# Kernel optimization log

Hardware: AMD Instinct MI355X
Metric: run time of the kernel (lower is better)

Reference implementation:

```python
import jax, jax.numpy as jnp
import numpy as np
import math

H = 16  # heads
EPS_NORM = 1e-12
EPS_W = 1e-6


def setup_inputs() -> dict:
    key = jax.random.key(0)
    ks = jax.random.split(key, 6)
    B, T, d = 2, 2048, 1024
    s = 1.0 / math.sqrt(d)
    return {
        "x": jax.random.normal(ks[0], (B, T, d), dtype=jnp.float32),
        "Wq": jax.random.normal(ks[1], (d, d), dtype=jnp.float32) * s,
        "Wk": jax.random.normal(ks[2], (d, d), dtype=jnp.float32) * s,
        "Wv": jax.random.normal(ks[3], (d, d), dtype=jnp.float32) * s,
        "Wo": jax.random.normal(ks[4], (d, d), dtype=jnp.float32) * s,
        "bo": jnp.zeros((d,), dtype=jnp.float32),
    }


def _l2norm(t):
    # F.normalize(dim=-1): x / max(||x||, eps)
    n = jnp.sqrt(jnp.sum(t * t, axis=-1, keepdims=True))
    return t / jnp.maximum(n, EPS_NORM)


def reference(x, Wq, Wk, Wv, Wo, bo):
    B, T, d = x.shape
    dk = d // H
    # projections (torch Linear: y = x @ W.T), split heads -> [B, H, T, dk]
    def proj(W):
        return (x @ W.T).reshape(B, T, H, dk).transpose(0, 2, 1, 3)
    Q = _l2norm(proj(Wq))
    K = _l2norm(proj(Wk))
    V = proj(Wv)
    # angular similarity scores [B, H, T, T]
    sim = jnp.clip(jnp.einsum("bhqd,bhkd->bhqk", Q, K), -0.999, 0.999)
    scores = 1.0 - jnp.arccos(sim) / jnp.float32(math.pi)
    W = jnp.maximum(scores, EPS_W) ** 8
    W = W / (jnp.sum(W, axis=-1, keepdims=True) + EPS_W)
    out = jnp.einsum("bhqk,bhkd->bhqd", W, V)  # [B, H, T, dk]
    out = out.transpose(0, 2, 1, 3).reshape(B, T, d)
    return out @ Wo.T + bo
```

## Files before the change

kernel.cpp:

```cpp
#include <hip/hip_runtime.h>
#include <hip/hip_bf16.h>
#include <hip/hip_fp16.h>
#include <math.h>

#define BB 2
#define TT 2048
#define DD 1024
#define HH 16
#define DK 64
#define KT 64

typedef _Float16 f16x8 __attribute__((ext_vector_type(8)));
typedef __fp16 fp16x2 __attribute__((ext_vector_type(2)));
typedef __attribute__((ext_vector_type(4))) float f32x4;
typedef __attribute__((ext_vector_type(2))) float f32x2;

static __device__ __forceinline__ void g2lds16(const void* g, void* l) {
    __builtin_amdgcn_global_load_lds(
        (const __attribute__((address_space(1))) unsigned int*)g,
        (__attribute__((address_space(3))) unsigned int*)l, 16, 0, 0);
}

static __device__ __forceinline__ f32x2 w8pair(f32x2 s, f32x2& rs) {
    f32x2 ax;
    ax.x = fminf(fabsf(s.x), 0.999f);
    ax.y = fminf(fabsf(s.y), 0.999f);
    f32x2 p = ax * -0.0059617f + 0.0236380f;
    p = p * ax + (-0.0675180f);
    p = p * ax + 0.49997851f;
    f32x2 om = 1.0f - ax;
    f32x2 u;
    u.x = sqrtf(om.x);
    u.y = sqrtf(om.y);
    f32x2 uq = u * p;
    f32x2 e = 0.5f - uq;
    f32x2 t;
    t.x = 0.5f + copysignf(e.x, s.x);
    t.y = 0.5f + copysignf(e.y, s.y);
    f32x2 t2 = t * t;
    f32x2 t4 = t2 * t2;
    f32x2 t8 = t4 * t4;
    rs += t8;
    return t8;
}
static __device__ __forceinline__ int packh2(f32x2 v) {
    union { fp16x2 h; int i; } u;
    u.h = __builtin_amdgcn_cvt_pkrtz(v.x, v.y);
    return u.i;
}

__global__ __launch_bounds__(256) void cvtall_kernel(
    const float* __restrict__ x,  const float* __restrict__ Wq,
    const float* __restrict__ Wk, const float* __restrict__ Wv,
    const float* __restrict__ Wo,
    _Float16* __restrict__ xh, _Float16* __restrict__ W3h,
    _Float16* __restrict__ Woh)
{
    const int bid = blockIdx.x;
    const float* s; _Float16* d; int blk;
    if (bid < 2048) { s = x; d = xh; blk = bid; }
    else {
        const int idx = bid - 2048;
        const int w   = idx >> 9;
        blk = idx & 511;
        s = (w == 0) ? Wq : (w == 1) ? Wk : (w == 2) ? Wv : Wo;
        d = (w == 3) ? Woh : W3h + (size_t)w * (DD * DD);
    }
    const int i = (blk * 256 + threadIdx.x) * 8;
    float4 a = *(const float4*)(s + i);
    float4 b = *(const float4*)(s + i + 4);
    union { _Float16 h[8]; int4 v; } u;
    u.h[0] = (_Float16)a.x; u.h[1] = (_Float16)a.y;
    u.h[2] = (_Float16)a.z; u.h[3] = (_Float16)a.w;
    u.h[4] = (_Float16)b.x; u.h[5] = (_Float16)b.y;
    u.h[6] = (_Float16)b.z; u.h[7] = (_Float16)b.w;
    *(int4*)(d + i) = u.v;
}

template<int NPROD, int EPI>
__global__ __launch_bounds__(256, NPROD == 1 ? 3 : 2) void gemm_f16_128(
    const _Float16* __restrict__ Ah_g, const _Float16* __restrict__ Al_g,
    const _Float16* __restrict__ B_g, const float* __restrict__ bias,
    float* __restrict__ C,
    _Float16* __restrict__ Qh, _Float16* __restrict__ Kh,
    _Float16* __restrict__ Vh,
    int nbx, int K, int hasBias)
{
    __shared__ _Float16 Ahs[8][128][8];
    __shared__ _Float16 Bhs[8][128][8];
    __shared__ _Float16 Als[NPROD == 2 ? 8 : 1][128][8];

    const int nwg  = gridDim.x;
    const int wgid = blockIdx.x;
    const int cpx  = nwg >> 3;
    const int swz  = (wgid & 7) * cpx + (wgid >> 3);
    const int by   = swz / nbx;
    const int bx   = swz - by * nbx;

    const int t    = threadIdx.x;
    const int m0   = by * 128;
    const int n0g  = bx * 128;
    const int seg  = n0g >> 10;
    const int n0   = n0g & 1023;

    const int lane = t & 63;
    const int w    = t >> 6;
    const int wm   = w >> 1;
    const int wn   = w & 1;
    const int l15  = lane & 15;
    const int quad = lane >> 4;

    f32x4 acc[4][4];
#pragma unroll
    for (int i = 0; i < 4; ++i)
#pragma unroll
        for (int j = 0; j < 4; ++j) acc[i][j] = (f32x4)0.f;

    for (int k0 = 0; k0 < K; k0 += 64) {
        __syncthreads();
#pragma unroll
        for (int i = 0; i < 2; ++i) {
            const int cc = w * 2 + i;
#pragma unroll
            for (int half = 0; half < 2; ++half) {
                g2lds16(Ah_g + (size_t)(m0 + half * 64 + lane) * K + k0 + cc * 8,
                        &Ahs[cc][half * 64][0]);
                if (NPROD == 2)
                    g2lds16(Al_g + (size_t)(m0 + half * 64 + lane) * K + k0 + cc * 8,
                            &Als[cc][half * 64][0]);
                g2lds16(B_g + (size_t)(n0g + half * 64 + lane) * K + k0 + cc * 8,
                        &Bhs[cc][half * 64][0]);
            }
        }
        __syncthreads();

#pragma unroll
        for (int kh = 0; kh < 2; ++kh) {
            f16x8 ah[4], bh[4];
#pragma unroll
            for (int tm = 0; tm < 4; ++tm)
                ah[tm] = *(const f16x8*)&Ahs[kh * 4 + quad][wm * 64 + tm * 16 + l15][0];
#pragma unroll
            for (int tn = 0; tn < 4; ++tn)
                bh[tn] = *(const f16x8*)&Bhs[kh * 4 + quad][wn * 64 + tn * 16 + l15][0];
#pragma unroll
            for (int tm = 0; tm < 4; ++tm)
#pragma unroll
                for (int tn = 0; tn < 4; ++tn)
                    acc[tm][tn] = __builtin_amdgcn_mfma_f32_16x16x32_f16(
                        ah[tm], bh[tn], acc[tm][tn], 0, 0, 0);
            if (NPROD == 2) {
                f16x8 al[4];
#pragma unroll
                for (int tm = 0; tm < 4; ++tm)
                    al[tm] = *(const f16x8*)&Als[kh * 4 + quad][wm * 64 + tm * 16 + l15][0];
#pragma unroll
                for (int tm = 0; tm < 4; ++tm)
#pragma unroll
                    for (int tn = 0; tn < 4; ++tn)
                        acc[tm][tn] = __builtin_amdgcn_mfma_f32_16x16x32_f16(
                            al[tm], bh[tn], acc[tm][tn], 0, 0, 0);
            }
        }
    }

    if (EPI == 0) {
#pragma unroll
        for (int tm = 0; tm < 4; ++tm)
#pragma unroll
            for (int tn = 0; tn < 4; ++tn) {
                const int col  = n0 + wn * 64 + tn * 16 + l15;
                const float bv = hasBias ? bias[col] : 0.f;
                const int rowb = m0 + wm * 64 + tm * 16 + quad * 4;
#pragma unroll
                for (int r = 0; r < 4; ++r)
                    C[(size_t)(rowb + r) * 1024 + col] = acc[tm][tn][r] + bv;
            }
    } else {
        if (seg < 2) {
            _Float16* __restrict__ dstb = (seg == 0) ? Qh : Kh;
            const int hh = (n0 >> 6) + wn;
#pragma unroll
            for (int tm = 0; tm < 4; ++tm) {
#pragma unroll
                for (int r = 0; r < 4; ++r) {
                    float ss = 0.f;
#pragma unroll
                    for (int tn = 0; tn < 4; ++tn) {
                        const float v = acc[tm][tn][r];
                        ss += v * v;
                    }
                    ss += __shfl_xor(ss, 1);
                    ss += __shfl_xor(ss, 2);
                    ss += __shfl_xor(ss, 4);
                    ss += __shfl_xor(ss, 8);
                    const float inv = rsqrtf(fmaxf(ss, 1e-24f));
                    const int row = m0 + wm * 64 + tm * 16 + quad * 4 + r;
                    const int b   = row >> 11;
                    const int tt  = row & 2047;
                    _Float16* dst = dstb + ((size_t)(b * HH + hh) * TT + tt) * DK;
#pragma unroll
                    for (int tn = 0; tn < 4; ++tn)
                        dst[tn * 16 + l15] = (_Float16)(acc[tm][tn][r] * inv);
                }
            }
        } else {
#pragma unroll
            for (int tm = 0; tm < 4; ++tm)
#pragma unroll
                for (int tn = 0; tn < 4; ++tn) {
                    const int col  = n0 + wn * 64 + tn * 16 + l15;
                    const int rowb = m0 + wm * 64 + tm * 16 + quad * 4;
#pragma unroll
                    for (int r = 0; r < 4; ++r)
                        Vh[(size_t)(rowb + r) * 1024 + col] =
                            (_Float16)acc[tm][tn][r];
                }
        }
    }
}

__global__ __launch_bounds__(256) void vtrans_kernel(
    const _Float16* __restrict__ Vh, _Float16* __restrict__ Vt)
{
    __shared__ _Float16 Vtmp[64][72];
    const int t  = threadIdx.x;
    const int t0 = blockIdx.x * 64;
    const int h  = blockIdx.y;
    const int b  = blockIdx.z;

    {
        const int i  = t >> 2;
        const int jc = (t & 3) * 16;
        const _Float16* src = Vh + (size_t)(b * TT + t0 + i) * DD + h * DK + jc;
        f16x8 a = *(const f16x8*)(src);
        f16x8 c = *(const f16x8*)(src + 8);
#pragma unroll
        for (int e = 0; e < 8; ++e) {
            Vtmp[jc + e][i]     = a[e];
            Vtmp[jc + 8 + e][i] = c[e];
        }
    }
    __syncthreads();
    {
        const int d  = t >> 2;
        const int kc = (t & 3) * 16;
        _Float16* dst = Vt + ((size_t)((b * HH + h) * DK + d)) * TT + t0 + kc;
        *(int4*)(dst)     = *(const int4*)&Vtmp[d][kc];
        *(int4*)(dst + 8) = *(const int4*)&Vtmp[d][kc + 8];
    }
}

__global__ __launch_bounds__(256, 4) void attn_kernel(
    const _Float16* __restrict__ Qh_g, const _Float16* __restrict__ Kh_g,
    const _Float16* __restrict__ Vt_g,
    _Float16* __restrict__ Oh, _Float16* __restrict__ Ol)
{
    __shared__ _Float16 Vts[2][8][64][8];
    __shared__ _Float16 Ws[2][64][72];
    __shared__ float Rbuf[4][64];
    __shared__ float Rfin[64];

    const int t    = threadIdx.x;
    const int lane = t & 63;
    const int w    = t >> 6;
    const int l15  = lane & 15;
    const int quad = lane >> 4;
    const int q0   = blockIdx.x * 64;
    const int h    = blockIdx.y;
    const int b    = blockIdx.z;
    const size_t bh = (size_t)(b * HH + h);

    const _Float16* kh_g = Kh_g + bh * TT * DK;
    const _Float16* vt_g = Vt_g + bh * (size_t)DK * TT;

    f16x8 qf[4][2];
#pragma unroll
    for (int qt = 0; qt < 4; ++qt)
#pragma unroll
        for (int s = 0; s < 2; ++s)
            qf[qt][s] = *(const f16x8*)(Qh_g + (bh * TT + q0 + qt * 16 + l15) * DK
                                        + s * 32 + quad * 8);

    f16x8 kf[2], kfn[2];
#pragma unroll
    for (int s = 0; s < 2; ++s) {
        kf[s] = *(const f16x8*)(kh_g
            + (size_t)(w * 16 + l15) * DK + s * 32 + quad * 8);
        kfn[s] = kf[s];
    }

#pragma unroll
    for (int j = 0; j < 2; ++j) {
        const int kc = w * 2 + j;
        g2lds16(vt_g + (size_t)lane * TT + kc * 8, &Vts[0][kc][0][0]);
    }

    f32x4 acc[4];
#pragma unroll
    for (int j = 0; j < 4; ++j) acc[j] = (f32x4)0.f;
    f32x2 rs2[4];
#pragma unroll
    for (int j = 0; j < 4; ++j) rs2[j] = (f32x2)0.f;

    int p = 0;
    for (int k0 = 0; k0 < TT; k0 += KT, p ^= 1) {
        const int kn = k0 + KT;
        if (kn < TT) {
#pragma unroll
            for (int s = 0; s < 2; ++s)
                kfn[s] = *(const f16x8*)(kh_g
                    + (size_t)(kn + w * 16 + l15) * DK + s * 32 + quad * 8);
        }

#pragma unroll
        for (int qt = 0; qt < 4; ++qt) {
            f32x4 c_ = (f32x4)0.f;
#pragma unroll
            for (int s = 0; s < 2; ++s)
                c_ = __builtin_amdgcn_mfma_f32_16x16x32_f16(
                    kf[s], qf[qt][s], c_, 0, 0, 0);
            f32x2 p01, p23;
            p01.x = c_[0]; p01.y = c_[1];
            p23.x = c_[2]; p23.y = c_[3];
            f32x2 w01 = w8pair(p01, rs2[qt]);
            f32x2 w23 = w8pair(p23, rs2[qt]);
            int2 pk;
            pk.x = packh2(w01);
            pk.y = packh2(w23);
            *(int2*)&Ws[p][qt * 16 + l15][w * 16 + quad * 4] = pk;
        }
        __syncthreads();

        if (kn < TT) {
#pragma unroll
            for (int j = 0; j < 2; ++j) {
                const int kc = w * 2 + j;
                g2lds16(vt_g + (size_t)lane * TT + kn + kc * 8,
                        &Vts[p ^ 1][kc][0][0]);
            }
        }

#pragma unroll
        for (int kstep = 0; kstep < 2; ++kstep) {
            f16x8 av = *(const f16x8*)&Ws[p][16 * w + l15][kstep * 32 + quad * 8];
#pragma unroll
            for (int nd = 0; nd < 4; ++nd) {
                f16x8 bv = *(const f16x8*)&Vts[p][kstep * 4 + quad][nd * 16 + l15][0];
                acc[nd] = __builtin_amdgcn_mfma_f32_16x16x32_f16(
                    av, bv, acc[nd], 0, 0, 0);
            }
        }

#pragma unroll
        for (int s = 0; s < 2; ++s)
            kf[s] = kfn[s];
    }

#pragma unroll
    for (int qt = 0; qt < 4; ++qt) {
        float pr = rs2[qt].x + rs2[qt].y;
        pr += __shfl_xor(pr, 16);
        pr += __shfl_xor(pr, 32);
        if (quad == 0) Rbuf[w][qt * 16 + l15] = pr;
    }
    __syncthreads();
    if (t < 64) {
        float s = Rbuf[0][t] + Rbuf[1][t] + Rbuf[2][t] + Rbuf[3][t];
        Rfin[t] = 1.f / (s + 1e-6f);
    }
    __syncthreads();

#pragma unroll
    for (int r = 0; r < 4; ++r) {
        const int q = 16 * w + quad * 4 + r;
        const float inv = Rfin[q];
        const size_t base = (size_t)(b * TT + q0 + q) * DD + h * DK + l15;
#pragma unroll
        for (int nd = 0; nd < 4; ++nd) {
            float v = acc[nd][r] * inv;
            _Float16 hv = (_Float16)v;
            Oh[base + nd * 16] = hv;
            Ol[base + nd * 16] = (_Float16)(v - (float)hv);
        }
    }
}

extern "C" void kernel_launch(void* const* d_in, const int* in_sizes, int n_in,
                              void* d_out, int out_size, void* d_ws, size_t ws_size,
                              hipStream_t stream)
{
    const float* x  = (const float*)d_in[0];
    const float* Wq = (const float*)d_in[1];
    const float* Wk = (const float*)d_in[2];
    const float* Wv = (const float*)d_in[3];
    const float* Wo = (const float*)d_in[4];
    const float* bo = (const float*)d_in[5];
    float* out = (float*)d_out;

    const int M = BB * TT;
    const int K = DD;

    const size_t MB = 1024 * 1024;
    char* ws = (char*)d_ws;
    _Float16* xh  = (_Float16*)(ws);
    _Float16* W3h = (_Float16*)(ws + 8 * MB);
    _Float16* Woh = (_Float16*)(ws + 14 * MB);
    _Float16* Qh  = (_Float16*)(ws + 16 * MB);
    _Float16* Kh  = (_Float16*)(ws + 24 * MB);
    _Float16* Vh  = (_Float16*)(ws + 32 * MB);
    _Float16* Vt  = (_Float16*)(ws + 40 * MB);
    _Float16* Oh  = (_Float16*)(ws);
    _Float16* Ol  = (_Float16*)(ws + 32 * MB);

    dim3 gB(256);

    cvtall_kernel<<<4096, gB, 0, stream>>>(x, Wq, Wk, Wv, Wo, xh, W3h, Woh);

    {
        const int nbx = 3072 / 128;
        const int nby = M / 128;
        gemm_f16_128<1, 1><<<nbx * nby, gB, 0, stream>>>(
            xh, nullptr, W3h, nullptr, nullptr, Qh, Kh, Vh, nbx, K, 0);
    }

    vtrans_kernel<<<dim3(TT / 64, HH, BB), gB, 0, stream>>>(Vh, Vt);

    attn_kernel<<<dim3(TT / 64, HH, BB), gB, 0, stream>>>(Qh, Kh, Vt, Oh, Ol);

    {
        const int nbx = 1024 / 128;
        const int nby = M / 128;
        gemm_f16_128<2, 0><<<nbx * nby, gB, 0, stream>>>(
            Oh, Ol, Woh, bo, out, nullptr, nullptr, nullptr, nbx, K, 1);
    }
}
```

Before: 310.8 us.

## Fuse V transpose into QKV GEMM epilogue and fold hi/lo split into K=2048 GEMM

The QKV GEMM epilogue now writes V directly in transposed [b,h,d,t] layout, so the separate vtrans kernel and the Vh buffer are gone. The attention output hi/lo fp16 halves are stored side by side in one [M,2048] buffer, and Wo is duplicated along K. The output projection becomes a single-product GEMM with K=2048 instead of a dual-A-operand variant. sqrt and rsqrt calls are also replaced with the AMDGCN builtins. The trade-offs are strided 8-byte V stores, twice the Wo fp16 storage, and possibly different occupancy for the output GEMM now that it uses 3 waves per SIMD.

```diff
diff --git a/kernel.cpp b/kernel.cpp
--- a/kernel.cpp
+++ b/kernel.cpp
@@ -30,8 +30,8 @@
     p = p * ax + 0.49997851f;
     f32x2 om = 1.0f - ax;
     f32x2 u;
-    u.x = sqrtf(om.x);
-    u.y = sqrtf(om.y);
+    u.x = __builtin_amdgcn_sqrtf(om.x);
+    u.y = __builtin_amdgcn_sqrtf(om.y);
     f32x2 uq = u * p;
     f32x2 e = 0.5f - uq;
     f32x2 t;
@@ -54,17 +54,16 @@
     const float* __restrict__ Wk, const float* __restrict__ Wv,
     const float* __restrict__ Wo,
     _Float16* __restrict__ xh, _Float16* __restrict__ W3h,
-    _Float16* __restrict__ Woh)
+    _Float16* __restrict__ Wo2)
 {
     const int bid = blockIdx.x;
-    const float* s; _Float16* d; int blk;
-    if (bid < 2048) { s = x; d = xh; blk = bid; }
+    const float* s; int wsel = -1, blk;
+    if (bid < 2048) { s = x; blk = bid; }
     else {
         const int idx = bid - 2048;
-        const int w   = idx >> 9;
-        blk = idx & 511;
-        s = (w == 0) ? Wq : (w == 1) ? Wk : (w == 2) ? Wv : Wo;
-        d = (w == 3) ? Woh : W3h + (size_t)w * (DD * DD);
+        wsel = idx >> 9;
+        blk  = idx & 511;
+        s = (wsel == 0) ? Wq : (wsel == 1) ? Wk : (wsel == 2) ? Wv : Wo;
     }
     const int i = (blk * 256 + threadIdx.x) * 8;
     float4 a = *(const float4*)(s + i);
@@ -74,21 +73,26 @@
     u.h[2] = (_Float16)a.z; u.h[3] = (_Float16)a.w;
     u.h[4] = (_Float16)b.x; u.h[5] = (_Float16)b.y;
     u.h[6] = (_Float16)b.z; u.h[7] = (_Float16)b.w;
-    *(int4*)(d + i) = u.v;
-}
-
-template<int NPROD, int EPI>
-__global__ __launch_bounds__(256, NPROD == 1 ? 3 : 2) void gemm_f16_128(
-    const _Float16* __restrict__ Ah_g, const _Float16* __restrict__ Al_g,
-    const _Float16* __restrict__ B_g, const float* __restrict__ bias,
-    float* __restrict__ C,
+    if (wsel < 0)      *(int4*)(xh + i) = u.v;
+    else if (wsel < 3) *(int4*)(W3h + (size_t)wsel * (DD * DD) + i) = u.v;
+    else {
+        const int n = i >> 10, k = i & 1023;
+        _Float16* dst = Wo2 + (size_t)n * 2048 + k;
+        *(int4*)dst          = u.v;
+        *(int4*)(dst + 1024) = u.v;
+    }
+}
+
+template<int EPI>
+__global__ __launch_bounds__(256, 3) void gemm_f16_128(
+    const _Float16* __restrict__ Ah_g, const _Float16* __restrict__ B_g,
+    const float* __restrict__ bias, float* __restrict__ C,
     _Float16* __restrict__ Qh, _Float16* __restrict__ Kh,
-    _Float16* __restrict__ Vh,
+    _Float16* __restrict__ Vt,
     int nbx, int K, int hasBias)
 {
     __shared__ _Float16 Ahs[8][128][8];
     __shared__ _Float16 Bhs[8][128][8];
-    __shared__ _Float16 Als[NPROD == 2 ? 8 : 1][128][8];
 
     const int nwg  = gridDim.x;
     const int wgid = blockIdx.x;
@@ -125,9 +129,6 @@
             for (int half = 0; half < 2; ++half) {
                 g2lds16(Ah_g + (size_t)(m0 + half * 64 + lane) * K + k0 + cc * 8,
                         &Ahs[cc][half * 64][0]);
-                if (NPROD == 2)
-                    g2lds16(Al_g + (size_t)(m0 + half * 64 + lane) * K + k0 + cc * 8,
-                            &Als[cc][half * 64][0]);
                 g2lds16(B_g + (size_t)(n0g + half * 64 + lane) * K + k0 + cc * 8,
                         &Bhs[cc][half * 64][0]);
             }
@@ -149,18 +150,6 @@
                 for (int tn = 0; tn < 4; ++tn)
                     acc[tm][tn] = __builtin_amdgcn_mfma_f32_16x16x32_f16(
                         ah[tm], bh[tn], acc[tm][tn], 0, 0, 0);
-            if (NPROD == 2) {
-                f16x8 al[4];
-#pragma unroll
-                for (int tm = 0; tm < 4; ++tm)
-                    al[tm] = *(const f16x8*)&Als[kh * 4 + quad][wm * 64 + tm * 16 + l15][0];
-#pragma unroll
-                for (int tm = 0; tm < 4; ++tm)
-#pragma unroll
-                    for (int tn = 0; tn < 4; ++tn)
-                        acc[tm][tn] = __builtin_amdgcn_mfma_f32_16x16x32_f16(
-                            al[tm], bh[tn], acc[tm][tn], 0, 0, 0);
-            }
         }
     }
 
@@ -194,7 +183,7 @@
                     ss += __shfl_xor(ss, 2);
                     ss += __shfl_xor(ss, 4);
                     ss += __shfl_xor(ss, 8);
-                    const float inv = rsqrtf(fmaxf(ss, 1e-24f));
+                    const float inv = __builtin_amdgcn_rsqf(fmaxf(ss, 1e-24f));
                     const int row = m0 + wm * 64 + tm * 16 + quad * 4 + r;
                     const int b   = row >> 11;
                     const int tt  = row & 2047;
@@ -205,56 +194,31 @@
                 }
             }
         } else {
-#pragma unroll
-            for (int tm = 0; tm < 4; ++tm)
-#pragma unroll
-                for (int tn = 0; tn < 4; ++tn) {
-                    const int col  = n0 + wn * 64 + tn * 16 + l15;
-                    const int rowb = m0 + wm * 64 + tm * 16 + quad * 4;
-#pragma unroll
-                    for (int r = 0; r < 4; ++r)
-                        Vh[(size_t)(rowb + r) * 1024 + col] =
-                            (_Float16)acc[tm][tn][r];
+            const int hh = (n0 >> 6) + wn;
+            const int rowb = m0 + wm * 64 + quad * 4;
+            const int bb  = rowb >> 11;
+            const int tt0 = rowb & 2047;
+#pragma unroll
+            for (int tn = 0; tn < 4; ++tn) {
+                const int d = tn * 16 + l15;
+                _Float16* dst = Vt + ((size_t)(bb * HH + hh) * DK + d) * TT;
+#pragma unroll
+                for (int tm = 0; tm < 4; ++tm) {
+                    union { _Float16 h[4]; int2 v; } uu;
+                    uu.h[0] = (_Float16)acc[tm][tn][0];
+                    uu.h[1] = (_Float16)acc[tm][tn][1];
+                    uu.h[2] = (_Float16)acc[tm][tn][2];
+                    uu.h[3] = (_Float16)acc[tm][tn][3];
+                    *(int2*)(dst + tt0 + tm * 16) = uu.v;
                 }
-        }
-    }
-}
-
-__global__ __launch_bounds__(256) void vtrans_kernel(
-    const _Float16* __restrict__ Vh, _Float16* __restrict__ Vt)
-{
-    __shared__ _Float16 Vtmp[64][72];
-    const int t  = threadIdx.x;
-    const int t0 = blockIdx.x * 64;
-    const int h  = blockIdx.y;
-    const int b  = blockIdx.z;
-
-    {
-        const int i  = t >> 2;
-        const int jc = (t & 3) * 16;
-        const _Float16* src = Vh + (size_t)(b * TT + t0 + i) * DD + h * DK + jc;
-        f16x8 a = *(const f16x8*)(src);
-        f16x8 c = *(const f16x8*)(src + 8);
-#pragma unroll
-        for (int e = 0; e < 8; ++e) {
-            Vtmp[jc + e][i]     = a[e];
-            Vtmp[jc + 8 + e][i] = c[e];
-        }
-    }
-    __syncthreads();
-    {
-        const int d  = t >> 2;
-        const int kc = (t & 3) * 16;
-        _Float16* dst = Vt + ((size_t)((b * HH + h) * DK + d)) * TT + t0 + kc;
-        *(int4*)(dst)     = *(const int4*)&Vtmp[d][kc];
-        *(int4*)(dst + 8) = *(const int4*)&Vtmp[d][kc + 8];
+            }
+        }
     }
 }
 
 __global__ __launch_bounds__(256, 4) void attn_kernel(
     const _Float16* __restrict__ Qh_g, const _Float16* __restrict__ Kh_g,
-    const _Float16* __restrict__ Vt_g,
-    _Float16* __restrict__ Oh, _Float16* __restrict__ Ol)
+    const _Float16* __restrict__ Vt_g, _Float16* __restrict__ O2)
 {
     __shared__ _Float16 Vts[2][8][64][8];
     __shared__ _Float16 Ws[2][64][72];
@@ -375,13 +339,13 @@
     for (int r = 0; r < 4; ++r) {
         const int q = 16 * w + quad * 4 + r;
         const float inv = Rfin[q];
-        const size_t base = (size_t)(b * TT + q0 + q) * DD + h * DK + l15;
+        const size_t base = (size_t)(b * TT + q0 + q) * 2048 + h * DK + l15;
 #pragma unroll
         for (int nd = 0; nd < 4; ++nd) {
             float v = acc[nd][r] * inv;
             _Float16 hv = (_Float16)v;
-            Oh[base + nd * 16] = hv;
-            Ol[base + nd * 16] = (_Float16)(v - (float)hv);
+            O2[base + nd * 16]        = hv;
+            O2[base + 1024 + nd * 16] = (_Float16)(v - (float)hv);
         }
     }
 }
@@ -399,39 +363,34 @@
     float* out = (float*)d_out;
 
     const int M = BB * TT;
-    const int K = DD;
 
     const size_t MB = 1024 * 1024;
     char* ws = (char*)d_ws;
     _Float16* xh  = (_Float16*)(ws);
     _Float16* W3h = (_Float16*)(ws + 8 * MB);
-    _Float16* Woh = (_Float16*)(ws + 14 * MB);
-    _Float16* Qh  = (_Float16*)(ws + 16 * MB);
-    _Float16* Kh  = (_Float16*)(ws + 24 * MB);
-    _Float16* Vh  = (_Float16*)(ws + 32 * MB);
+    _Float16* Wo2 = (_Float16*)(ws + 16 * MB);
+    _Float16* Qh  = (_Float16*)(ws + 24 * MB);
+    _Float16* Kh  = (_Float16*)(ws + 32 * MB);
     _Float16* Vt  = (_Float16*)(ws + 40 * MB);
-    _Float16* Oh  = (_Float16*)(ws);
-    _Float16* Ol  = (_Float16*)(ws + 32 * MB);
+    _Float16* O2  = (_Float16*)(ws);
 
     dim3 gB(256);
 
-    cvtall_kernel<<<4096, gB, 0, stream>>>(x, Wq, Wk, Wv, Wo, xh, W3h, Woh);
+    cvtall_kernel<<<4096, gB, 0, stream>>>(x, Wq, Wk, Wv, Wo, xh, W3h, Wo2);
 
     {
         const int nbx = 3072 / 128;
         const int nby = M / 128;
-        gemm_f16_128<1, 1><<<nbx * nby, gB, 0, stream>>>(
-            xh, nullptr, W3h, nullptr, nullptr, Qh, Kh, Vh, nbx, K, 0);
-    }
-
-    vtrans_kernel<<<dim3(TT / 64, HH, BB), gB, 0, stream>>>(Vh, Vt);
-
-    attn_kernel<<<dim3(TT / 64, HH, BB), gB, 0, stream>>>(Qh, Kh, Vt, Oh, Ol);
+        gemm_f16_128<1><<<nbx * nby, gB, 0, stream>>>(
+            xh, W3h, nullptr, nullptr, Qh, Kh, Vt, nbx, DD, 0);
+    }
+
+    attn_kernel<<<dim3(TT / 64, HH, BB), gB, 0, stream>>>(Qh, Kh, Vt, O2);
 
     {
         const int nbx = 1024 / 128;
         const int nby = M / 128;
-        gemm_f16_128<2, 0><<<nbx * nby, gB, 0, stream>>>(
-            Oh, Ol, Woh, bo, out, nullptr, nullptr, nullptr, nbx, K, 1);
-    }
-}
+        gemm_f16_128<0><<<nbx * nby, gB, 0, stream>>>(
+            O2, Wo2, bo, out, nullptr, nullptr, nullptr, nbx, 2048, 1);
+    }
+}
```

New measurement: 279.1 us. 10.2% less time.
